# Optimization experiments

Hardware: AMD Instinct MI355X
Metric: run time of the kernel (lower is better)

The kernel has to match this reference:

```python
import jax, jax.numpy as jnp
import numpy as np

B, S, D, H = 2, 2048, 1024, 16
DK = D // H
NEG = -1e9


def setup_inputs() -> dict:
    key = jax.random.key(0)
    ks = jax.random.split(key, 11)
    s = 1.0 / np.sqrt(D)
    inp = {
        "q": jax.random.normal(ks[0], (B, S, D), jnp.float32),
        "k": jax.random.normal(ks[1], (B, S, D), jnp.float32),
        "v": jax.random.normal(ks[2], (B, S, D), jnp.float32),
        "mask": jnp.tril(jnp.ones((S, S), jnp.int32))[None, None],  # [1,1,S,S] causal
        "Wq": jax.random.normal(ks[3], (D, D), jnp.float32) * s,
        "bq": jnp.zeros((D,), jnp.float32),
        "Wk": jax.random.normal(ks[4], (D, D), jnp.float32) * s,
        "bk": jnp.zeros((D,), jnp.float32),
        "Wv": jax.random.normal(ks[5], (D, D), jnp.float32) * s,
        "bv": jnp.zeros((D,), jnp.float32),
        "Wo": jax.random.normal(ks[6], (D, D), jnp.float32) * s,
        "bo": jnp.zeros((D,), jnp.float32),
    }
    return inp


def reference(q, k, v, mask, Wq, bq, Wk, bk, Wv, bv, Wo, bo):
    # projections (torch Linear: x @ W.T + b)
    Q = q @ Wq.T + bq
    K = k @ Wk.T + bk
    V = v @ Wv.T + bv
    # [B,S,D] -> [B,H,S,DK]
    Q = Q.reshape(B, S, H, DK).transpose(0, 2, 1, 3)
    K = K.reshape(B, S, H, DK).transpose(0, 2, 1, 3)
    V = V.reshape(B, S, H, DK).transpose(0, 2, 1, 3)
    scores = jnp.einsum("bhqd,bhkd->bhqk", Q, K) / jnp.sqrt(jnp.float32(DK))
    scores = jnp.where(mask == 0, jnp.float32(NEG), scores)
    attn = jax.nn.softmax(scores, axis=-1)  # dropout p=0.0 -> identity
    x = jnp.einsum("bhqk,bhkd->bhqd", attn, V)
    x = x.transpose(0, 2, 1, 3).reshape(B, S, D)
    return x @ Wo.T + bo
```

## Files before the change

### kernel.cpp

```cpp
#include <hip/hip_runtime.h>
#include <hip/hip_bf16.h>


typedef __bf16 bf16_t;
typedef __bf16 bf16x4 __attribute__((ext_vector_type(4)));
typedef __bf16 bf16x8 __attribute__((ext_vector_type(8)));
typedef float f32x4 __attribute__((ext_vector_type(4)));

#define BB 2
#define SS 2048
#define DD 1024
#define HH 16
#define DKK 64
#define MM 4096

#define NELT ((size_t)BB * SS * DD)
#define WELT ((size_t)DD * DD)

__device__ __align__(16) bf16_t g_ws[4 * NELT + 4 * WELT];

__device__ __forceinline__ void gld16(const bf16_t* g, bf16_t* l) {
    __builtin_amdgcn_global_load_lds(
        (const __attribute__((address_space(1))) void*)g,
        (__attribute__((address_space(3))) void*)l, 16, 0, 0);
}

__global__ __launch_bounds__(256) void cvt_w(
    const float* __restrict__ Wq, const float* __restrict__ Wk,
    const float* __restrict__ Wv, const float* __restrict__ Wo,
    bf16_t* __restrict__ Wqb, bf16_t* __restrict__ Wkb,
    bf16_t* __restrict__ Wvb, bf16_t* __restrict__ Wob)
{
    const float* s; bf16_t* d;
    switch (blockIdx.y) {
        case 0:  s = Wq; d = Wqb; break;
        case 1:  s = Wk; d = Wkb; break;
        case 2:  s = Wv; d = Wvb; break;
        default: s = Wo; d = Wob; break;
    }
    size_t e = ((size_t)blockIdx.x * 256 + threadIdx.x) * 8;
    if (e >= WELT) return;
    f32x4 a = *(const f32x4*)(s + e);
    f32x4 b = *(const f32x4*)(s + e + 4);
    bf16x8 o;
    #pragma unroll
    for (int i = 0; i < 4; ++i) { o[i] = (bf16_t)a[i]; o[4 + i] = (bf16_t)b[i]; }
    *(bf16x8*)(d + e) = o;
}

#define BMQ 64
#define BNQ 128
#define BKG 64
#define LDCQ 68

__global__ __launch_bounds__(256) void gemm_qkv5(
    const float* __restrict__ qf32, const float* __restrict__ kf32, const float* __restrict__ vf32,
    const bf16_t* __restrict__ Wqb, const bf16_t* __restrict__ Wkb, const bf16_t* __restrict__ Wvb,
    const float* __restrict__ bq, const float* __restrict__ bk, const float* __restrict__ bv,
    bf16_t* __restrict__ Qp, bf16_t* __restrict__ Kp, bf16_t* __restrict__ Vt)
{
    const int z = blockIdx.z;
    const float*  A    = (z == 0) ? qf32 : (z == 1) ? kf32 : vf32;
    const bf16_t* W    = (z == 0) ? Wqb  : (z == 1) ? Wkb  : Wvb;
    const float*  bias = (z == 0) ? bq   : (z == 1) ? bk   : bv;

    __shared__ __align__(16) bf16_t smem[(BMQ + BNQ) * BKG];
    bf16_t (*As)[BKG]  = (bf16_t(*)[BKG])smem;
    bf16_t (*Bs)[BKG]  = (bf16_t(*)[BKG])(smem + BMQ * BKG);
    bf16_t (*Ct)[LDCQ] = (bf16_t(*)[LDCQ])smem;

    const int tid  = threadIdx.x;
    const int wave = tid >> 6;
    const int lane = tid & 63;
    const int quad = lane >> 4;
    const int c16  = lane & 15;

    const int f  = blockIdx.x + 64 * blockIdx.y;
    const int f2 = (f & 7) * 64 + (f >> 3);
    const int bm = (f2 >> 3) * BMQ;
    const int bn = (f2 & 7) * BNQ;

    const int wm = (wave >> 1) * 32;
    const int wn = (wave & 1) * 64;

    const int srow = lane >> 3;
    const int scol = (lane & 7) * 8;

    f32x4 acc[2][4] = {};

    for (int k0 = 0; k0 < DD; k0 += BKG) {
        __syncthreads();
        #pragma unroll
        for (int j = 0; j < 2; ++j) {
            int r0 = wave * 16 + j * 8;
            const float* ap = A + (size_t)(bm + r0 + srow) * DD + k0 + scol;
            f32x4 x = *(const f32x4*)ap;
            f32x4 y = *(const f32x4*)(ap + 4);
            bf16x8 o;
            #pragma unroll
            for (int i = 0; i < 4; ++i) { o[i] = (bf16_t)x[i]; o[4 + i] = (bf16_t)y[i]; }
            *(bf16x8*)(&As[r0 + srow][scol]) = o;
        }
        #pragma unroll
        for (int j = 0; j < 4; ++j) {
            int r0 = wave * 32 + j * 8;
            gld16(W + (size_t)(bn + r0 + srow) * DD + k0 + scol, &Bs[r0][0]);
        }
        __syncthreads();

        #pragma unroll
        for (int ks = 0; ks < 2; ++ks) {
            bf16x8 af[2], bfr[4];
            #pragma unroll
            for (int tm = 0; tm < 2; ++tm)
                af[tm] = *(const bf16x8*)(&As[wm + tm * 16 + c16][ks * 32 + quad * 8]);
            #pragma unroll
            for (int tn = 0; tn < 4; ++tn)
                bfr[tn] = *(const bf16x8*)(&Bs[wn + tn * 16 + c16][ks * 32 + quad * 8]);
            #pragma unroll
            for (int tm = 0; tm < 2; ++tm)
                #pragma unroll
                for (int tn = 0; tn < 4; ++tn)
                    acc[tm][tn] = __builtin_amdgcn_mfma_f32_16x16x32_bf16(
                        af[tm], bfr[tn], acc[tm][tn], 0, 0, 0);
        }
    }

    float bia[4];
    #pragma unroll
    for (int tn = 0; tn < 4; ++tn)
        bia[tn] = bias[bn + wn + tn * 16 + c16];

    if (z < 2) {
        const float osc = (z == 0) ? 0.125f * 1.4426950408889634f : 1.0f;
        bf16_t* C = (z == 0) ? Qp : Kp;
        #pragma unroll
        for (int tm = 0; tm < 2; ++tm)
            #pragma unroll
            for (int r = 0; r < 4; ++r) {
                size_t base = (size_t)(bm + wm + tm * 16 + quad * 4 + r) * DD;
                #pragma unroll
                for (int tn = 0; tn < 4; ++tn)
                    C[base + bn + wn + tn * 16 + c16] =
                        (bf16_t)((acc[tm][tn][r] + bia[tn]) * osc);
            }
    } else {
        __syncthreads();
        #pragma unroll
        for (int tm = 0; tm < 2; ++tm)
            #pragma unroll
            for (int tn = 0; tn < 4; ++tn) {
                bf16x4 pk;
                #pragma unroll
                for (int r = 0; r < 4; ++r)
                    pk[r] = (bf16_t)(acc[tm][tn][r] + bia[tn]);
                *(bf16x4*)(&Ct[wn + tn * 16 + c16][wm + tm * 16 + quad * 4]) = pk;
            }
        __syncthreads();
        const int b_    = bm >> 11;
        const int sbase = bm & (SS - 1);
        #pragma unroll
        for (int p = 0; p < 4; ++p) {
            int col = p * 32 + (tid >> 3);
            int si  = (tid & 7) * 8;
            size_t rowoff = (size_t)(b_ * 1024 + bn + col) * SS + sbase;
            *(bf16x8*)(&Vt[rowoff + si]) = *(const bf16x8*)(&Ct[col][si]);
        }
    }
}

__global__ __launch_bounds__(256) void gemm_out(
    const bf16_t* __restrict__ A,
    const bf16_t* __restrict__ W,
    const float* __restrict__ bias,
    float* __restrict__ C)
{
    __shared__ __align__(16) bf16_t As[64][BKG];
    __shared__ __align__(16) bf16_t Bs[64][BKG];

    const int tid  = threadIdx.x;
    const int wave = tid >> 6;
    const int lane = tid & 63;
    const int quad = lane >> 4;
    const int c16  = lane & 15;

    const int f  = blockIdx.x + 64 * blockIdx.y;
    const int f2 = (f & 7) * 128 + (f >> 3);
    const int bm = (f2 >> 4) * 64;
    const int bn = (f2 & 15) * 64;

    const int wm = (wave >> 1) * 32;
    const int wn = (wave & 1) * 32;

    const int srow = lane >> 3;
    const int scol = (lane & 7) * 8;

    f32x4 acc[2][2] = {};

    for (int k0 = 0; k0 < DD; k0 += BKG) {
        __syncthreads();
        #pragma unroll
        for (int j = 0; j < 2; ++j) {
            int r0 = wave * 16 + j * 8;
            gld16(A + (size_t)(bm + r0 + srow) * DD + k0 + scol, &As[r0][0]);
            gld16(W + (size_t)(bn + r0 + srow) * DD + k0 + scol, &Bs[r0][0]);
        }
        __syncthreads();

        #pragma unroll
        for (int ks = 0; ks < 2; ++ks) {
            bf16x8 af[2], bfr[2];
            #pragma unroll
            for (int tm = 0; tm < 2; ++tm)
                af[tm] = *(const bf16x8*)(&As[wm + tm * 16 + c16][ks * 32 + quad * 8]);
            #pragma unroll
            for (int tn = 0; tn < 2; ++tn)
                bfr[tn] = *(const bf16x8*)(&Bs[wn + tn * 16 + c16][ks * 32 + quad * 8]);
            #pragma unroll
            for (int tm = 0; tm < 2; ++tm)
                #pragma unroll
                for (int tn = 0; tn < 2; ++tn)
                    acc[tm][tn] = __builtin_amdgcn_mfma_f32_16x16x32_bf16(
                        af[tm], bfr[tn], acc[tm][tn], 0, 0, 0);
        }
    }

    float bia[2];
    #pragma unroll
    for (int tn = 0; tn < 2; ++tn)
        bia[tn] = bias[bn + wn + tn * 16 + c16];

    #pragma unroll
    for (int tm = 0; tm < 2; ++tm)
        #pragma unroll
        for (int r = 0; r < 4; ++r) {
            size_t base = (size_t)(bm + wm + tm * 16 + quad * 4 + r) * DD;
            #pragma unroll
            for (int tn = 0; tn < 2; ++tn)
                C[base + bn + wn + tn * 16 + c16] = acc[tm][tn][r] + bia[tn];
        }
}

#define LDPS 40
#define LDCF 68

#define LOADK(KF, UU)                                                          \
do {                                                                           \
    const int kb_ = (UU) * 32;                                                 \
    const bf16_t* kp0 = Kb + (size_t)(kb_ + c16) * DD;                         \
    const bf16_t* kp1 = Kb + (size_t)(kb_ + 16 + c16) * DD;                    \
    KF[0][0] = *(const bf16x8*)(kp0 + quad * 8);                               \
    KF[0][1] = *(const bf16x8*)(kp0 + 32 + quad * 8);                          \
    KF[1][0] = *(const bf16x8*)(kp1 + quad * 8);                               \
    KF[1][1] = *(const bf16x8*)(kp1 + 32 + quad * 8);                          \
} while (0)

#define ATTN_STEP(UU, KFC, KFN)                                                \
do {                                                                           \
    const int kb_ = (UU) * 32;                                                 \
    f32x4 sc_[2][2];                                                           \
    __builtin_amdgcn_s_setprio(1);                                             \
    _Pragma("unroll")                                                          \
    for (int tm = 0; tm < 2; ++tm)                                             \
        _Pragma("unroll")                                                      \
        for (int ct = 0; ct < 2; ++ct) {                                       \
            f32x4 s_ = {};                                                     \
            s_ = __builtin_amdgcn_mfma_f32_16x16x32_bf16(                      \
                     KFC[ct][0], qf[tm][0], s_, 0, 0, 0);                      \
            s_ = __builtin_amdgcn_mfma_f32_16x16x32_bf16(                      \
                     KFC[ct][1], qf[tm][1], s_, 0, 0, 0);                      \
            sc_[tm][ct] = s_;                                                  \
        }                                                                      \
    __builtin_amdgcn_s_setprio(0);                                             \
    if ((UU) + 4 < U) LOADK(KFN, (UU) + 4);                                    \
    bf16x8 vf_[4];                                                             \
    _Pragma("unroll")                                                          \
    for (int tn = 0; tn < 4; ++tn)                                             \
        vf_[tn] = *(const bf16x8*)(Vb + (size_t)(tn * 16 + c16) * SS           \
                                   + kb_ + quad * 8);                          \
    const bool needmask_ = (kb_ == qbase);                                     \
    _Pragma("unroll")                                                          \
    for (int tm = 0; tm < 2; ++tm) {                                           \
        const int qrow_ = qbase + tm * 16 + c16;                               \
        _Pragma("unroll")                                                      \
        for (int ct = 0; ct < 2; ++ct) {                                       \
            bf16x4 w_;                                                         \
            _Pragma("unroll")                                                  \
            for (int r = 0; r < 4; ++r) {                                      \
                float s_ = sc_[tm][ct][r];                                     \
                if (needmask_ && (kb_ + ct * 16 + quad * 4 + r > qrow_))       \
                    s_ = -1e9f;                                                \
                float p_ = __builtin_amdgcn_exp2f(s_);                         \
                lsum2[tm] += p_;                                               \
                w_[r] = (bf16_t)p_;                                            \
            }                                                                  \
            *(bf16x4*)(pw + tm * 16 * LDPS + ct * 16) = w_;                    \
        }                                                                      \
    }                                                                          \
    asm volatile("s_waitcnt lgkmcnt(0)" ::: "memory");                         \
    __builtin_amdgcn_s_setprio(1);                                             \
    _Pragma("unroll")                                                          \
    for (int tm = 0; tm < 2; ++tm) {                                           \
        bf16x8 pa_ = *(const bf16x8*)(pr + tm * 16 * LDPS);                    \
        _Pragma("unroll")                                                      \
        for (int tn = 0; tn < 4; ++tn)                                         \
            oacc[tm][tn] = __builtin_amdgcn_mfma_f32_16x16x32_bf16(            \
                pa_, vf_[tn], oacc[tm][tn], 0, 0, 0);                          \
    }                                                                          \
    __builtin_amdgcn_s_setprio(0);                                             \
} while (0)

__global__ __launch_bounds__(256) void attn_fwd11(
    const bf16_t* __restrict__ Q,
    const bf16_t* __restrict__ K,
    const bf16_t* __restrict__ Vt,
    bf16_t* __restrict__ O)
{
    const int flat = blockIdx.x;
    const int bh   = (flat & 7) * 4 + (flat >> 8);
    const int pair = (flat >> 3) & 31;
    const int b = bh >> 4;
    const int h = bh & 15;

    const int wave = threadIdx.x >> 6;
    const int lane = threadIdx.x & 63;
    const int quad = lane >> 4;
    const int c16  = lane & 15;

    __shared__ __align__(16) unsigned char smraw[4 * 16 * LDCF * 4];
    bf16_t (*Ps)[32][LDPS] = (bf16_t(*)[32][LDPS])smraw;
    float  (*Cf)[16][LDCF] = (float(*)[16][LDCF])smraw;
    __shared__ float Ls[4][32];

    const bf16_t* Kb = K  + (size_t)b * SS * DD + h * DKK;
    const bf16_t* Vb = Vt + (size_t)(b * 1024 + h * DKK) * SS;

    bf16_t*       pw = &Ps[wave][c16][quad * 4];
    const bf16_t* pr = &Ps[wave][c16][quad * 8];

    for (int t = 0; t < 2; ++t) {
        const int qt    = (t == 0) ? (63 - pair) : pair;
        const int qbase = qt * 32;
        const int U     = qt + 1;

        bf16x8 qf[2][2];
        #pragma unroll
        for (int tm = 0; tm < 2; ++tm) {
            const bf16_t* qp = Q + ((size_t)b * SS + qbase + tm * 16 + c16) * DD + h * DKK;
            qf[tm][0] = *(const bf16x8*)(qp + quad * 8);
            qf[tm][1] = *(const bf16x8*)(qp + 32 + quad * 8);
        }

        f32x4 oacc[2][4] = {};
        float lsum2[2] = {0.f, 0.f};

        bf16x8 kfA[2][2], kfB[2][2];

        {
            int u = wave;
            if (u < U) {
                LOADK(kfA, u);
                for (;;) {
                    ATTN_STEP(u, kfA, kfB); u += 4;
                    if (u >= U) break;
                    ATTN_STEP(u, kfB, kfA); u += 4;
                    if (u >= U) break;
                }
            }
        }

        #pragma unroll
        for (int tm = 0; tm < 2; ++tm) {
            float l = lsum2[tm];
            l += __shfl_xor(l, 16, 64);
            l += __shfl_xor(l, 32, 64);
            if (lane < 16) Ls[wave][tm * 16 + lane] = l;
        }

        const int row = threadIdx.x >> 4;
        const int col = (threadIdx.x & 15) * 4;
        #pragma unroll
        for (int tm = 0; tm < 2; ++tm) {
            __syncthreads();
            #pragma unroll
            for (int tn = 0; tn < 4; ++tn)
                #pragma unroll
                for (int r = 0; r < 4; ++r)
                    Cf[wave][quad * 4 + r][tn * 16 + c16] = oacc[tm][tn][r];
            __syncthreads();
            f32x4 ssum = {};
            #pragma unroll
            for (int p = 0; p < 4; ++p)
                ssum += *(const f32x4*)(&Cf[p][row][col]);
            float l = Ls[0][tm * 16 + row] + Ls[1][tm * 16 + row]
                    + Ls[2][tm * 16 + row] + Ls[3][tm * 16 + row];
            float inv = 1.0f / l;
            bf16x4 o;
            #pragma unroll
            for (int i = 0; i < 4; ++i) o[i] = (bf16_t)(ssum[i] * inv);
            *(bf16x4*)(&O[((size_t)b * SS + qbase + tm * 16 + row) * DD + h * DKK + col]) = o;
        }
        __syncthreads();
    }
}

extern "C" void kernel_launch(void* const* d_in, const int* in_sizes, int n_in,
                              void* d_out, int out_size, void* d_ws, size_t ws_size,
                              hipStream_t stream) {
    (void)in_sizes; (void)n_in; (void)out_size; (void)d_ws; (void)ws_size;
    const float* q  = (const float*)d_in[0];
    const float* k  = (const float*)d_in[1];
    const float* v  = (const float*)d_in[2];
    const float* Wq = (const float*)d_in[4];
    const float* bq = (const float*)d_in[5];
    const float* Wk = (const float*)d_in[6];
    const float* bk = (const float*)d_in[7];
    const float* Wv = (const float*)d_in[8];
    const float* bv = (const float*)d_in[9];
    const float* Wo = (const float*)d_in[10];
    const float* bo = (const float*)d_in[11];

    bf16_t* ws;
    hipGetSymbolAddress((void**)&ws, HIP_SYMBOL(g_ws));
    bf16_t* Qp  = ws;
    bf16_t* Kp  = Qp + NELT;
    bf16_t* Vt  = Kp + NELT;
    bf16_t* Xa  = Vt + NELT;
    bf16_t* Wqb = Xa + NELT;
    bf16_t* Wkb = Wqb + WELT;
    bf16_t* Wvb = Wkb + WELT;
    bf16_t* Wob = Wvb + WELT;

    cvt_w<<<dim3(512, 4), 256, 0, stream>>>(Wq, Wk, Wv, Wo,
                                            Wqb, Wkb, Wvb, Wob);

    gemm_qkv5<<<dim3(MM / BMQ, DD / BNQ, 3), 256, 0, stream>>>(
        q, k, v, Wqb, Wkb, Wvb, bq, bk, bv, Qp, Kp, Vt);

    attn_fwd11<<<dim3(1024), 256, 0, stream>>>(Qp, Kp, Vt, Xa);

    gemm_out<<<dim3(64, 16), 256, 0, stream>>>(Xa, Wob, bo, (float*)d_out);
}
```

Before: 284.5 us.

## Prefetch next fp32 A tile into registers and XOR-swizzle A in LDS

The QKV projection GEMM now issues the global loads for the next k-step's fp32 activation tile into registers right after the barrier. Those loads overlap with the MFMA work of the current tile, hiding global latency that was previously exposed at the start of each iteration. The bf16 A tile in shared memory is also stored and read with an XOR swizzle to reduce LDS bank conflicts on the fragment reads. The cost is extra registers for the prefetch buffer, which may lower occupancy.

```diff
diff --git a/kernel.cpp b/kernel.cpp
--- a/kernel.cpp
+++ b/kernel.cpp
@@ -53,7 +53,33 @@
 #define BKG 64
 #define LDCQ 68
 
-__global__ __launch_bounds__(256) void gemm_qkv5(
+#define LOADA(K0)                                                              \
+do {                                                                           \
+    _Pragma("unroll")                                                          \
+    for (int j = 0; j < 2; ++j) {                                              \
+        int r0 = wave * 16 + j * 8;                                            \
+        const float* ap = A + (size_t)(bm + r0 + srow) * DD + (K0) + scol;     \
+        ax[j] = *(const f32x4*)ap;                                             \
+        ay[j] = *(const f32x4*)(ap + 4);                                       \
+    }                                                                          \
+} while (0)
+
+#define WRITEA()                                                               \
+do {                                                                           \
+    _Pragma("unroll")                                                          \
+    for (int j = 0; j < 2; ++j) {                                              \
+        int r0 = wave * 16 + j * 8;                                            \
+        bf16x8 o;                                                              \
+        _Pragma("unroll")                                                      \
+        for (int i = 0; i < 4; ++i) {                                          \
+            o[i] = (bf16_t)ax[j][i]; o[4 + i] = (bf16_t)ay[j][i];              \
+        }                                                                      \
+        *(bf16x8*)(&As[0][0] + (size_t)(r0 + srow) * BKG                       \
+                   + (scol ^ (srow << 3))) = o;                                \
+    }                                                                          \
+} while (0)
+
+__global__ __launch_bounds__(256) void gemm_qkv6(
     const float* __restrict__ qf32, const float* __restrict__ kf32, const float* __restrict__ vf32,
     const bf16_t* __restrict__ Wqb, const bf16_t* __restrict__ Wkb, const bf16_t* __restrict__ Wvb,
     const float* __restrict__ bq, const float* __restrict__ bk, const float* __restrict__ bv,
@@ -85,22 +111,15 @@
 
     const int srow = lane >> 3;
     const int scol = (lane & 7) * 8;
+    const int swzA = (c16 & 7) << 3;
 
     f32x4 acc[2][4] = {};
-
+    f32x4 ax[2], ay[2];
+
+    LOADA(0);
     for (int k0 = 0; k0 < DD; k0 += BKG) {
         __syncthreads();
-        #pragma unroll
-        for (int j = 0; j < 2; ++j) {
-            int r0 = wave * 16 + j * 8;
-            const float* ap = A + (size_t)(bm + r0 + srow) * DD + k0 + scol;
-            f32x4 x = *(const f32x4*)ap;
-            f32x4 y = *(const f32x4*)(ap + 4);
-            bf16x8 o;
-            #pragma unroll
-            for (int i = 0; i < 4; ++i) { o[i] = (bf16_t)x[i]; o[4 + i] = (bf16_t)y[i]; }
-            *(bf16x8*)(&As[r0 + srow][scol]) = o;
-        }
+        WRITEA();
         #pragma unroll
         for (int j = 0; j < 4; ++j) {
             int r0 = wave * 32 + j * 8;
@@ -108,12 +127,16 @@
         }
         __syncthreads();
 
+        if (k0 + BKG < DD) LOADA(k0 + BKG);
+
         #pragma unroll
         for (int ks = 0; ks < 2; ++ks) {
             bf16x8 af[2], bfr[4];
             #pragma unroll
             for (int tm = 0; tm < 2; ++tm)
-                af[tm] = *(const bf16x8*)(&As[wm + tm * 16 + c16][ks * 32 + quad * 8]);
+                af[tm] = *(const bf16x8*)(&As[0][0]
+                    + (size_t)(wm + tm * 16 + c16) * BKG
+                    + ((ks * 32 + quad * 8) ^ swzA));
             #pragma unroll
             for (int tn = 0; tn < 4; ++tn)
                 bfr[tn] = *(const bf16x8*)(&Bs[wn + tn * 16 + c16][ks * 32 + quad * 8]);
@@ -434,7 +457,7 @@
     cvt_w<<<dim3(512, 4), 256, 0, stream>>>(Wq, Wk, Wv, Wo,
                                             Wqb, Wkb, Wvb, Wob);
 
-    gemm_qkv5<<<dim3(MM / BMQ, DD / BNQ, 3), 256, 0, stream>>>(
+    gemm_qkv6<<<dim3(MM / BMQ, DD / BNQ, 3), 256, 0, stream>>>(
         q, k, v, Wqb, Wkb, Wvb, bq, bk, bv, Qp, Kp, Vt);
 
     attn_fwd11<<<dim3(1024), 256, 0, stream>>>(Qp, Kp, Vt, Xa);
```

Measured after the change: 268.6 us. -5.6%, faster.
